# Kernel optimization log

Hardware: AMD Instinct MI355X
Metric: run time of the kernel (lower is better)

## Reference

```python
import jax, jax.numpy as jnp
import numpy as np

POOL_H, POOL_W = 7, 7


def _crop_and_resize_one(feat, boxes, pool_h, pool_w):
    """TF crop_and_resize-style bilinear sampling.
    feat: [H, W, C]; boxes: [N, 4] normalized (y1, x1, y2, x2).
    Returns [N, pool_h, pool_w, C].
    """
    H, W, C = feat.shape
    y1, x1, y2, x2 = boxes[:, 0], boxes[:, 1], boxes[:, 2], boxes[:, 3]
    fy = jnp.arange(pool_h, dtype=feat.dtype) / (pool_h - 1)  # [ph] in [0,1]
    fx = jnp.arange(pool_w, dtype=feat.dtype) / (pool_w - 1)  # [pw]
    ys = (y1[:, None] + fy[None, :] * (y2 - y1)[:, None]) * (H - 1)  # [N, ph]
    xs = (x1[:, None] + fx[None, :] * (x2 - x1)[:, None]) * (W - 1)  # [N, pw]
    y0f = jnp.clip(jnp.floor(ys), 0, H - 1)
    x0f = jnp.clip(jnp.floor(xs), 0, W - 1)
    y0 = y0f.astype(jnp.int32)
    x0 = x0f.astype(jnp.int32)
    y1i = jnp.clip(y0 + 1, 0, H - 1)
    x1i = jnp.clip(x0 + 1, 0, W - 1)
    wy = (ys - y0f)[:, :, None, None]  # [N, ph, 1, 1]
    wx = (xs - x0f)[:, None, :, None]  # [N, 1, pw, 1]
    # four corner gathers -> [N, ph, pw, C]
    f00 = feat[y0[:, :, None], x0[:, None, :]]
    f01 = feat[y0[:, :, None], x1i[:, None, :]]
    f10 = feat[y1i[:, :, None], x0[:, None, :]]
    f11 = feat[y1i[:, :, None], x1i[:, None, :]]
    top = f00 + (f01 - f00) * wx
    bot = f10 + (f11 - f10) * wx
    return top + (bot - top) * wy


def setup_inputs() -> dict:
    key = jax.random.key(0)
    kf, kb = jax.random.split(key)
    B, H, W, C, N = 2, 64, 64, 256, 2000
    features = jax.random.normal(kf, (B, H, W, C), dtype=jnp.float32)
    p = jax.random.uniform(kb, (B, N, 4), dtype=jnp.float32)
    # ensure valid normalized boxes (y1<=y2, x1<=x2)
    rois = jnp.stack([
        jnp.minimum(p[..., 0], p[..., 2]),
        jnp.minimum(p[..., 1], p[..., 3]),
        jnp.maximum(p[..., 0], p[..., 2]),
        jnp.maximum(p[..., 1], p[..., 3]),
    ], axis=-1)
    return {"features": features, "rois": rois}


def reference(features, rois):
    # [B, N, 7, 7, C]
    return jax.vmap(lambda f, b: _crop_and_resize_one(f, b, POOL_H, POOL_W))(features, rois)
```

## Files before the change

### kernel.cpp

```cpp
#include <hip/hip_runtime.h>


#define POOL 7

typedef float vfloat4 __attribute__((ext_vector_type(4)));

__global__ __launch_bounds__(256) void roialign_kernel(
    const float* __restrict__ feat,
    const float* __restrict__ rois,
    float* __restrict__ out,
    int H, int W, int C4, int N, int blocks_per_batch)
{
    const int lane = threadIdx.x & 63;
    const int wid  = threadIdx.x >> 6;

    const int xcd  = blockIdx.x & 7;
    const int slot = blockIdx.x >> 3;
    const int b    = xcd >> 2;
    const int lblock = slot * 4 + (xcd & 3);
    if (lblock >= blocks_per_batch) return;

    const int row = lblock * 4 + wid;
    const int rows_per_batch = N * POOL;
    if (row >= rows_per_batch) return;

    const int n  = row / POOL;
    const int py = row - n * POOL;

    const float* r = rois + ((long long)b * N + n) * 4;
    const float ry1 = r[0], rx1 = r[1], ry2 = r[2], rx2 = r[3];

    const float fy = (float)py * (1.0f / (POOL - 1));
    const float ys = (ry1 + fy * (ry2 - ry1)) * (float)(H - 1);
    const float y0f = fminf(fmaxf(floorf(ys), 0.0f), (float)(H - 1));
    const int   y0  = (int)y0f;
    const int   y1i = min(y0 + 1, H - 1);
    const float wy  = ys - y0f;

    const vfloat4* fb = (const vfloat4*)feat + (long long)b * H * W * C4;
    const vfloat4* r0 = fb + (long long)y0  * W * C4 + lane;
    const vfloat4* r1 = fb + (long long)y1i * W * C4 + lane;

    vfloat4* ob = (vfloat4*)out +
                  (((long long)b * N + n) * (POOL * POOL) + (long long)py * POOL) * C4 + lane;

    const float dx = rx2 - rx1;

#pragma unroll
    for (int px = 0; px < POOL; ++px) {
        const float fx  = (float)px * (1.0f / (POOL - 1));
        const float xs  = (rx1 + fx * dx) * (float)(W - 1);
        const float x0f = fminf(fmaxf(floorf(xs), 0.0f), (float)(W - 1));
        const int   x0  = (int)x0f;
        const int   x1i = min(x0 + 1, W - 1);
        const float wx  = xs - x0f;

        const vfloat4 f00 = r0[x0  * C4];
        const vfloat4 f01 = r0[x1i * C4];
        const vfloat4 f10 = r1[x0  * C4];
        const vfloat4 f11 = r1[x1i * C4];

        const vfloat4 top = f00 + (f01 - f00) * wx;
        const vfloat4 bot = f10 + (f11 - f10) * wx;
        const vfloat4 o   = top + (bot - top) * wy;

        __builtin_nontemporal_store(o, ob + px * C4);
    }
}

extern "C" void kernel_launch(void* const* d_in, const int* in_sizes, int n_in,
                              void* d_out, int out_size, void* d_ws, size_t ws_size,
                              hipStream_t stream) {
    const int B = 2, H = 64, W = 64, C = 256;
    const int N = in_sizes[1] / (B * 4);

    const float* feat = (const float*)d_in[0];
    const float* rois = (const float*)d_in[1];
    float* out = (float*)d_out;

    const int rows_per_batch   = N * POOL;
    const int blocks_per_batch = (rows_per_batch + 3) / 4;
    const int slots  = (blocks_per_batch + 3) / 4;
    const int blocks = slots * 8;

    roialign_kernel<<<blocks, 256, 0, stream>>>(feat, rois, out,
                                                H, W, C / 4, N, blocks_per_batch);
}
```

Measured before the change: 216.2 us.

## Bin ROI rows by source feature row and stage rows in LDS

Adds a binning pass that groups output rows by batch and source y0 with atomics into workspace buckets. A new kernel then loads the two needed feature rows (128 KB) into LDS once per bin and serves all bilinear gathers from shared memory instead of global memory. It adds two extra launches, atomic contention, and large LDS use per block that limits occupancy. The direct kernel is kept as a fallback when the workspace is too small.

```diff
diff --git a/kernel.cpp b/kernel.cpp
--- a/kernel.cpp
+++ b/kernel.cpp
@@ -1,37 +1,139 @@
 #include <hip/hip_runtime.h>
 
 
-#define POOL 7
+#define POOL  7
+#define NBINS 128
+#define CAP   14000
+#define BPB   8
 
 typedef float vfloat4 __attribute__((ext_vector_type(4)));
 
-__global__ __launch_bounds__(256) void roialign_kernel(
+__global__ void zero_counts(int* __restrict__ counts) {
+    if ((int)threadIdx.x < NBINS) counts[threadIdx.x] = 0;
+}
+
+__global__ __launch_bounds__(256) void bin_rows(
+    const float* __restrict__ rois,
+    int* __restrict__ counts,
+    int* __restrict__ slots,
+    int H, int N)
+{
+    const int rows_per_batch = N * POOL;
+    const int total = 2 * rows_per_batch;
+    const int gid = blockIdx.x * 256 + threadIdx.x;
+    if (gid >= total) return;
+
+    const int b   = gid / rows_per_batch;
+    const int rem = gid - b * rows_per_batch;
+    const int n   = rem / POOL;
+    const int py  = rem - n * POOL;
+
+    const float* r = rois + ((long long)b * N + n) * 4;
+    const float ry1 = r[0], ry2 = r[2];
+
+    const float fy  = (float)py * (1.0f / (POOL - 1));
+    const float ys  = (ry1 + fy * (ry2 - ry1)) * (float)(H - 1);
+    const float y0f = fminf(fmaxf(floorf(ys), 0.0f), (float)(H - 1));
+    const int   y0  = (int)y0f;
+
+    const int bin = b * 64 + y0;
+    const int idx = atomicAdd(&counts[bin], 1);
+    slots[bin * CAP + idx] = rem;
+}
+
+__global__ __launch_bounds__(1024) void roialign_binned(
     const float* __restrict__ feat,
     const float* __restrict__ rois,
     float* __restrict__ out,
-    int H, int W, int C4, int N, int blocks_per_batch)
+    const int* __restrict__ counts,
+    const int* __restrict__ slots,
+    int H, int W, int C4, int N)
+{
+    __shared__ vfloat4 lds[2][64 * 64];
+
+    const int bin = blockIdx.x >> 3;
+    const int j   = blockIdx.x & (BPB - 1);
+    const int count = counts[bin];
+    const int s0 = (j * count) / BPB;
+    const int s1 = ((j + 1) * count) / BPB;
+    if (s0 >= s1) return;
+
+    const int b   = bin >> 6;
+    const int y0  = bin & 63;
+    const int y1i = min(y0 + 1, H - 1);
+
+    const vfloat4* fb = (const vfloat4*)feat + (long long)b * H * W * C4;
+    const vfloat4* g0 = fb + (long long)y0  * W * C4;
+    const vfloat4* g1 = fb + (long long)y1i * W * C4;
+    for (int t = threadIdx.x; t < W * C4; t += 1024) {
+        lds[0][t] = g0[t];
+        lds[1][t] = g1[t];
+    }
+    __syncthreads();
+
+    const int lane = threadIdx.x & 63;
+    const int wid  = threadIdx.x >> 6;
+
+    for (int i = s0 + wid; i < s1; i += 16) {
+        const int rem = slots[bin * CAP + i];
+        const int n   = rem / POOL;
+        const int py  = rem - n * POOL;
+
+        const float* r = rois + ((long long)b * N + n) * 4;
+        const float ry1 = r[0], rx1 = r[1], ry2 = r[2], rx2 = r[3];
+
+        const float fy  = (float)py * (1.0f / (POOL - 1));
+        const float ys  = (ry1 + fy * (ry2 - ry1)) * (float)(H - 1);
+        const float y0f = fminf(fmaxf(floorf(ys), 0.0f), (float)(H - 1));
+        const float wy  = ys - y0f;
+        const float dx  = rx2 - rx1;
+
+        vfloat4* ob = (vfloat4*)out +
+            (((long long)b * N + n) * (POOL * POOL) + (long long)py * POOL) * C4 + lane;
+
+#pragma unroll
+        for (int px = 0; px < POOL; ++px) {
+            const float fx  = (float)px * (1.0f / (POOL - 1));
+            const float xs  = (rx1 + fx * dx) * (float)(W - 1);
+            const float x0f = fminf(fmaxf(floorf(xs), 0.0f), (float)(W - 1));
+            const int   x0  = (int)x0f;
+            const int   x1i = min(x0 + 1, W - 1);
+            const float wx  = xs - x0f;
+
+            const vfloat4 f00 = lds[0][x0  * C4 + lane];
+            const vfloat4 f01 = lds[0][x1i * C4 + lane];
+            const vfloat4 f10 = lds[1][x0  * C4 + lane];
+            const vfloat4 f11 = lds[1][x1i * C4 + lane];
+
+            const vfloat4 top = f00 + (f01 - f00) * wx;
+            const vfloat4 bot = f10 + (f11 - f10) * wx;
+            const vfloat4 o   = top + (bot - top) * wy;
+
+            __builtin_nontemporal_store(o, ob + px * C4);
+        }
+    }
+}
+
+__global__ __launch_bounds__(256) void roialign_direct(
+    const float* __restrict__ feat, const float* __restrict__ rois,
+    float* __restrict__ out, int H, int W, int C4, int N, int blocks_per_batch)
 {
     const int lane = threadIdx.x & 63;
     const int wid  = threadIdx.x >> 6;
-
     const int xcd  = blockIdx.x & 7;
     const int slot = blockIdx.x >> 3;
     const int b    = xcd >> 2;
     const int lblock = slot * 4 + (xcd & 3);
     if (lblock >= blocks_per_batch) return;
-
     const int row = lblock * 4 + wid;
-    const int rows_per_batch = N * POOL;
-    if (row >= rows_per_batch) return;
-
+    if (row >= N * POOL) return;
     const int n  = row / POOL;
     const int py = row - n * POOL;
 
     const float* r = rois + ((long long)b * N + n) * 4;
     const float ry1 = r[0], rx1 = r[1], ry2 = r[2], rx2 = r[3];
-
-    const float fy = (float)py * (1.0f / (POOL - 1));
-    const float ys = (ry1 + fy * (ry2 - ry1)) * (float)(H - 1);
+    const float fy  = (float)py * (1.0f / (POOL - 1));
+    const float ys  = (ry1 + fy * (ry2 - ry1)) * (float)(H - 1);
     const float y0f = fminf(fmaxf(floorf(ys), 0.0f), (float)(H - 1));
     const int   y0  = (int)y0f;
     const int   y1i = min(y0 + 1, H - 1);
@@ -40,12 +142,9 @@
     const vfloat4* fb = (const vfloat4*)feat + (long long)b * H * W * C4;
     const vfloat4* r0 = fb + (long long)y0  * W * C4 + lane;
     const vfloat4* r1 = fb + (long long)y1i * W * C4 + lane;
-
     vfloat4* ob = (vfloat4*)out +
-                  (((long long)b * N + n) * (POOL * POOL) + (long long)py * POOL) * C4 + lane;
-
+        (((long long)b * N + n) * (POOL * POOL) + (long long)py * POOL) * C4 + lane;
     const float dx = rx2 - rx1;
-
 #pragma unroll
     for (int px = 0; px < POOL; ++px) {
         const float fx  = (float)px * (1.0f / (POOL - 1));
@@ -54,16 +153,13 @@
         const int   x0  = (int)x0f;
         const int   x1i = min(x0 + 1, W - 1);
         const float wx  = xs - x0f;
-
         const vfloat4 f00 = r0[x0  * C4];
         const vfloat4 f01 = r0[x1i * C4];
         const vfloat4 f10 = r1[x0  * C4];
         const vfloat4 f11 = r1[x1i * C4];
-
         const vfloat4 top = f00 + (f01 - f00) * wx;
         const vfloat4 bot = f10 + (f11 - f10) * wx;
         const vfloat4 o   = top + (bot - top) * wy;
-
         __builtin_nontemporal_store(o, ob + px * C4);
     }
 }
@@ -78,11 +174,25 @@
     const float* rois = (const float*)d_in[1];
     float* out = (float*)d_out;
 
-    const int rows_per_batch   = N * POOL;
-    const int blocks_per_batch = (rows_per_batch + 3) / 4;
-    const int slots  = (blocks_per_batch + 3) / 4;
-    const int blocks = slots * 8;
+    const size_t ws_needed = (size_t)NBINS * 4
+                           + (size_t)NBINS * CAP * 4;
 
-    roialign_kernel<<<blocks, 256, 0, stream>>>(feat, rois, out,
-                                                H, W, C / 4, N, blocks_per_batch);
+    if (ws_size >= ws_needed && d_ws != nullptr) {
+        int* counts = (int*)d_ws;
+        int* slots  = counts + NBINS;
+
+        const int total_rows = B * N * POOL;
+        const int bin_blocks = (total_rows + 255) / 256;
+
+        zero_counts<<<1, NBINS, 0, stream>>>(counts);
+        bin_rows<<<bin_blocks, 256, 0, stream>>>(rois, counts, slots, H, N);
+        roialign_binned<<<NBINS * BPB, 1024, 0, stream>>>(
+            feat, rois, out, counts, slots, H, W, C / 4, N);
+    } else {
+        const int rows_per_batch   = N * POOL;
+        const int blocks_per_batch = (rows_per_batch + 3) / 4;
+        const int slots_g  = (blocks_per_batch + 3) / 4;
+        roialign_direct<<<slots_g * 8, 256, 0, stream>>>(
+            feat, rois, out, H, W, C / 4, N, blocks_per_batch);
+    }
 }
```

Result: slower. 245.3 us (+13.4%).
